# Kernel tuning notes

Measured on AMD Instinct MI355X. Metric: run time of the kernel, lower is better.

Reference implementation:

```python
import jax, jax.numpy as jnp
import numpy as np

N = 50000
E = 800000
IN_F, HID, OUT_F = 512, 256, 64
BN_EPS = 1e-5


def setup_inputs() -> dict:
    key = jax.random.key(0)
    ks = jax.random.split(key, 8)
    x = jax.random.normal(ks[0], (N, IN_F), dtype=jnp.float32)
    edge_rows = jax.random.randint(ks[1], (E,), 0, N, dtype=jnp.int32)
    edge_cols = jax.random.randint(ks[2], (E,), 0, N, dtype=jnp.int32)
    edge_vals = jax.random.uniform(ks[3], (E,), dtype=jnp.float32)
    # xavier_uniform for weights, zeros for biases (as in the torch module)
    lim1 = float(np.sqrt(6.0 / (IN_F + HID)))
    lim2 = float(np.sqrt(6.0 / (HID + OUT_F)))
    W1 = jax.random.uniform(ks[4], (IN_F, HID), minval=-lim1, maxval=lim1, dtype=jnp.float32)
    b1 = jnp.zeros((HID,), dtype=jnp.float32)
    W2 = jax.random.uniform(ks[5], (HID, OUT_F), minval=-lim2, maxval=lim2, dtype=jnp.float32)
    b2 = jnp.zeros((OUT_F,), dtype=jnp.float32)
    # BatchNorm affine params (torch defaults: weight=1, bias=0)
    gamma1 = jnp.ones((HID,), dtype=jnp.float32)
    beta1 = jnp.zeros((HID,), dtype=jnp.float32)
    gamma2 = jnp.ones((OUT_F,), dtype=jnp.float32)
    beta2 = jnp.zeros((OUT_F,), dtype=jnp.float32)
    return dict(x=x, edge_rows=edge_rows, edge_cols=edge_cols, edge_vals=edge_vals,
                W1=W1, b1=b1, gamma1=gamma1, beta1=beta1,
                W2=W2, b2=b2, gamma2=gamma2, beta2=beta2)


def _spmm(rows, cols, vals, dense):
    # sparse [N,N] @ dense [N,F] via gather + segment-sum scatter
    msgs = vals[:, None] * dense[cols]            # [E, F]
    return jax.ops.segment_sum(msgs, rows, num_segments=N)


def _batchnorm(h, gamma, beta):
    # training-mode BatchNorm1d: batch statistics over nodes (biased var)
    mean = jnp.mean(h, axis=0)
    var = jnp.var(h, axis=0)
    return gamma * (h - mean) * jax.lax.rsqrt(var + BN_EPS) + beta


def reference(x, edge_rows, edge_cols, edge_vals,
              W1, b1, gamma1, beta1, W2, b2, gamma2, beta2):
    # layer 1: GCN conv -> BN -> ReLU (dropout is identity in eval / reference)
    h = _spmm(edge_rows, edge_cols, edge_vals, x @ W1) + b1
    h = jax.nn.relu(_batchnorm(h, gamma1, beta1))
    # layer 2: GCN conv -> BN -> log_softmax over classes
    h = _spmm(edge_rows, edge_cols, edge_vals, h @ W2) + b2
    h = _batchnorm(h, gamma2, beta2)
    return jax.nn.log_softmax(h, axis=1)
```

## Files before the change

kernel.cpp:

```cpp
#include <hip/hip_runtime.h>

typedef __attribute__((ext_vector_type(8))) short short8;
typedef __attribute__((ext_vector_type(4))) float f32x4;
typedef __attribute__((ext_vector_type(8))) unsigned short ushort8;

__device__ __forceinline__ unsigned short f2bf(float f) {
  unsigned int u = __builtin_bit_cast(unsigned int, f);
  u += 0x7fffu + ((u >> 16) & 1u);
  return (unsigned short)(u >> 16);
}
__device__ __forceinline__ float bf2f(unsigned short b) {
  return __builtin_bit_cast(float, ((unsigned int)b) << 16);
}
__device__ __forceinline__ void gload_lds16(const void* g, void* l) {
  __builtin_amdgcn_global_load_lds(
      (const __attribute__((address_space(1))) void*)g,
      (__attribute__((address_space(3))) void*)l, 16, 0, 0);
}

__global__ __launch_bounds__(256) void cvt_w1t(
    const float* __restrict__ W1, unsigned short* __restrict__ W1T)
{
  int idx = blockIdx.x * 256 + threadIdx.x;
  int n = idx >> 9, k = idx & 511;
  W1T[idx] = f2bf(W1[(size_t)k * 256 + n]);
}

__global__ __launch_bounds__(256) void cvt_w2t(
    const float* __restrict__ W2, unsigned short* __restrict__ W2T)
{
  int idx = blockIdx.x * 256 + threadIdx.x;
  int n = idx >> 8, k = idx & 255;
  W2T[idx] = f2bf(W2[(size_t)k * 64 + n]);
}

__global__ __launch_bounds__(256) void gemm1_mfma(
    const float* __restrict__ x,
    const unsigned short* __restrict__ w1t,
    unsigned short* __restrict__ H1,
    int M)
{
  __shared__ unsigned short As[2][64 * 64];
  __shared__ unsigned short Bs[2][256 * 64];
  const int tid = threadIdx.x;
  const int wid = tid >> 6, lane = tid & 63;
  const int wc = wid;
  const int m0 = blockIdx.x * 64;

  const int srow = tid >> 3;
  const int ls = ((tid & 7) ^ (srow & 7)) * 8;
  const unsigned short* gB = &w1t[(size_t)srow * 512 + ls];

  const int ar0 = tid >> 3;
  const int ar1 = ar0 + 32;
  const int ac  = tid & 7;
  const int arow0 = m0 + ar0;
  const int arow1 = m0 + ar1;

  float4 a0lo, a0hi, a1lo, a1hi;

  auto loadA = [&](int k0) {
    a0lo = make_float4(0.f, 0.f, 0.f, 0.f); a0hi = a0lo; a1lo = a0lo; a1hi = a0lo;
    if (arow0 < M) {
      a0lo = *(const float4*)&x[(size_t)arow0 * 512 + k0 + ac * 8];
      a0hi = *(const float4*)&x[(size_t)arow0 * 512 + k0 + ac * 8 + 4];
    }
    if (arow1 < M) {
      a1lo = *(const float4*)&x[(size_t)arow1 * 512 + k0 + ac * 8];
      a1hi = *(const float4*)&x[(size_t)arow1 * 512 + k0 + ac * 8 + 4];
    }
  };
  auto writeA = [&](int buf) {
    float v0[8] = {a0lo.x, a0lo.y, a0lo.z, a0lo.w, a0hi.x, a0hi.y, a0hi.z, a0hi.w};
    float v1[8] = {a1lo.x, a1lo.y, a1lo.z, a1lo.w, a1hi.x, a1hi.y, a1hi.z, a1hi.w};
    ushort8 o0, o1;
#pragma unroll
    for (int j = 0; j < 8; ++j) { o0[j] = f2bf(v0[j]); o1[j] = f2bf(v1[j]); }
    *(ushort8*)((char*)As[buf] + ar0 * 128 + ((ac ^ (ar0 & 7)) * 16)) = o0;
    *(ushort8*)((char*)As[buf] + ar1 * 128 + ((ac ^ (ar1 & 7)) * 16)) = o1;
  };
  auto stageB = [&](int k0, int buf) {
    char* lB = (char*)Bs[buf] + (size_t)wid * 1024;
#pragma unroll
    for (int i = 0; i < 8; ++i)
      gload_lds16(gB + (size_t)i * 32 * 512 + k0, lB + (size_t)i * 4096);
  };

  f32x4 acc[4][4] = {};

  loadA(0);
  stageB(0, 0);
  writeA(0);
  __syncthreads();

  for (int kt = 0; kt < 8; ++kt) {
    const int cur = kt & 1, nxt = cur ^ 1;
    if (kt < 7) {
      loadA((kt + 1) * 64);
      stageB((kt + 1) * 64, nxt);
    }
#pragma unroll
    for (int kk = 0; kk < 2; ++kk) {
      short8 a[4], b[4];
#pragma unroll
      for (int m = 0; m < 4; ++m) {
        int row = m * 16 + (lane & 15);
        int phys = (kk * 4 + (lane >> 4)) ^ (row & 7);
        a[m] = *(const short8*)((const char*)As[cur] + row * 128 + phys * 16);
      }
#pragma unroll
      for (int n = 0; n < 4; ++n) {
        int col = wc * 64 + n * 16 + (lane & 15);
        int phys = (kk * 4 + (lane >> 4)) ^ (col & 7);
        b[n] = *(const short8*)((const char*)Bs[cur] + col * 128 + phys * 16);
      }
#pragma unroll
      for (int m = 0; m < 4; ++m)
#pragma unroll
        for (int n = 0; n < 4; ++n)
          acc[m][n] = __builtin_amdgcn_mfma_f32_16x16x32_bf16(a[m], b[n], acc[m][n], 0, 0, 0);
    }
    if (kt < 7) writeA(nxt);
    __syncthreads();
  }

  const int colbase = wc * 64 + (lane & 15);
#pragma unroll
  for (int m = 0; m < 4; ++m) {
    int rowbase = m0 + m * 16 + (lane >> 4) * 4;
#pragma unroll
    for (int j = 0; j < 4; ++j) {
      int row = rowbase + j;
      if (row < M) {
#pragma unroll
        for (int n = 0; n < 4; ++n)
          H1[(size_t)row * 256 + colbase + n * 16] = f2bf(acc[m][n][j]);
      }
    }
  }
}

__global__ __launch_bounds__(256) void gemm2_mfma(
    const unsigned short* __restrict__ A,
    const unsigned short* __restrict__ w2t,
    const float* __restrict__ scsh,
    unsigned short* __restrict__ H2,
    int M)
{
  __shared__ unsigned short As[128 * 64];
  __shared__ unsigned short Bs[64 * 64];
  const int tid = threadIdx.x;
  const int wid = tid >> 6, lane = tid & 63;
  const int wr = wid >> 1, wc = wid & 1;
  const int m0 = blockIdx.x * 128;

  const int srow = tid >> 3;
  const int ls = ((tid & 7) ^ (srow & 7)) * 8;
  const unsigned short* gB = &w2t[(size_t)srow * 256 + ls];
  char* lB = (char*)Bs + (size_t)wid * 1024;

  f32x4 acc[4][2] = {};

  for (int kt = 0; kt < 4; ++kt) {
    const int k0 = kt * 64;
#pragma unroll
    for (int i = 0; i < 2; ++i)
      gload_lds16(gB + (size_t)i * 32 * 256 + k0, lB + (size_t)i * 4096);
#pragma unroll
    for (int i = 0; i < 4; ++i) {
      int chunk = tid + 256 * i;
      int r = chunk >> 3, c = chunk & 7;
      int gk = k0 + c * 8;
      ushort8 u = *(const ushort8*)&A[(size_t)(m0 + r) * 256 + gk];
      float4 sc0 = *(const float4*)&scsh[gk];
      float4 sc1 = *(const float4*)&scsh[gk + 4];
      float4 sh0 = *(const float4*)&scsh[256 + gk];
      float4 sh1 = *(const float4*)&scsh[256 + gk + 4];
      ushort8 o;
      o[0] = f2bf(fmaxf(bf2f(u[0]) * sc0.x + sh0.x, 0.f));
      o[1] = f2bf(fmaxf(bf2f(u[1]) * sc0.y + sh0.y, 0.f));
      o[2] = f2bf(fmaxf(bf2f(u[2]) * sc0.z + sh0.z, 0.f));
      o[3] = f2bf(fmaxf(bf2f(u[3]) * sc0.w + sh0.w, 0.f));
      o[4] = f2bf(fmaxf(bf2f(u[4]) * sc1.x + sh1.x, 0.f));
      o[5] = f2bf(fmaxf(bf2f(u[5]) * sc1.y + sh1.y, 0.f));
      o[6] = f2bf(fmaxf(bf2f(u[6]) * sc1.z + sh1.z, 0.f));
      o[7] = f2bf(fmaxf(bf2f(u[7]) * sc1.w + sh1.w, 0.f));
      *(ushort8*)((char*)As + r * 128 + ((c ^ (r & 7)) * 16)) = o;
    }
    __syncthreads();

#pragma unroll
    for (int kk = 0; kk < 2; ++kk) {
      short8 a[4], b[2];
#pragma unroll
      for (int m = 0; m < 4; ++m) {
        int row = wr * 64 + m * 16 + (lane & 15);
        int phys = (kk * 4 + (lane >> 4)) ^ (row & 7);
        a[m] = *(const short8*)((const char*)As + row * 128 + phys * 16);
      }
#pragma unroll
      for (int n = 0; n < 2; ++n) {
        int col = wc * 32 + n * 16 + (lane & 15);
        int phys = (kk * 4 + (lane >> 4)) ^ (col & 7);
        b[n] = *(const short8*)((const char*)Bs + col * 128 + phys * 16);
      }
#pragma unroll
      for (int m = 0; m < 4; ++m)
#pragma unroll
        for (int n = 0; n < 2; ++n)
          acc[m][n] = __builtin_amdgcn_mfma_f32_16x16x32_bf16(a[m], b[n], acc[m][n], 0, 0, 0);
    }
    __syncthreads();
  }

  const int colbase = wc * 32 + (lane & 15);
#pragma unroll
  for (int m = 0; m < 4; ++m) {
    int rowbase = m0 + wr * 64 + m * 16 + (lane >> 4) * 4;
#pragma unroll
    for (int j = 0; j < 4; ++j) {
      int row = rowbase + j;
      if (row < M) {
#pragma unroll
        for (int n = 0; n < 2; ++n)
          H2[(size_t)row * 64 + colbase + n * 16] = f2bf(acc[m][n][j]);
      }
    }
  }
}

__global__ __launch_bounds__(256) void edge_hist(
    const int* __restrict__ rows, int* __restrict__ cnt, int E)
{
  int e = blockIdx.x * 256 + threadIdx.x;
  if (e < E) atomicAdd(&cnt[rows[e]], 1);
}

__global__ __launch_bounds__(256) void scan_blocksum(
    const int* __restrict__ cnt, int* __restrict__ bsum, int Nrows)
{
  int i = blockIdx.x * 256 + threadIdx.x;
  int v = (i < Nrows) ? cnt[i] : 0;
#pragma unroll
  for (int off = 1; off < 64; off <<= 1) v += __shfl_xor(v, off);
  __shared__ int wsum[4];
  if ((threadIdx.x & 63) == 0) wsum[threadIdx.x >> 6] = v;
  __syncthreads();
  if (threadIdx.x == 0)
    bsum[blockIdx.x] = wsum[0] + wsum[1] + wsum[2] + wsum[3];
}

__global__ __launch_bounds__(256) void scan_boff(
    const int* __restrict__ bsum, int* __restrict__ boff, int NB)
{
  __shared__ int lds[256];
  int t = threadIdx.x;
  int v = (t < NB) ? bsum[t] : 0;
  lds[t] = v;
  __syncthreads();
  for (int off = 1; off < 256; off <<= 1) {
    int u = (t >= off) ? lds[t - off] : 0;
    __syncthreads();
    lds[t] += u;
    __syncthreads();
  }
  boff[t] = (t == 0) ? 0 : lds[t - 1];
}

__global__ __launch_bounds__(256) void scan_write(
    const int* __restrict__ cnt, const int* __restrict__ boff,
    int* __restrict__ rowptr, int* __restrict__ cursor, int Nrows, int E)
{
  __shared__ int lds[256];
  int t = threadIdx.x;
  int i = blockIdx.x * 256 + t;
  int v = (i < Nrows) ? cnt[i] : 0;
  lds[t] = v;
  __syncthreads();
  for (int off = 1; off < 256; off <<= 1) {
    int u = (t >= off) ? lds[t - off] : 0;
    __syncthreads();
    lds[t] += u;
    __syncthreads();
  }
  int excl = boff[blockIdx.x] + lds[t] - v;
  if (i < Nrows) { rowptr[i] = excl; cursor[i] = excl; }
  if (i == Nrows) rowptr[i] = E;
}

__global__ __launch_bounds__(256) void edge_scatter(
    const int* __restrict__ rows, const int* __restrict__ cols,
    const float* __restrict__ vals, int* __restrict__ cursor,
    int2* __restrict__ spack, int E)
{
  int e = blockIdx.x * 256 + threadIdx.x;
  if (e < E) {
    int r = rows[e];
    int p = atomicAdd(&cursor[r], 1);
    spack[p] = make_int2(cols[e], __float_as_int(vals[e]));
  }
}

__global__ __launch_bounds__(256) void spmm_gather_bf(
    const int* __restrict__ rowptr, const int2* __restrict__ sp,
    const unsigned short* __restrict__ D,
    unsigned short* __restrict__ out, int Nrows)
{
  const int lane = threadIdx.x & 63;
  const int r = blockIdx.x * 4 + (threadIdx.x >> 6);
  if (r >= Nrows) return;
  const int s = rowptr[r], e = rowptr[r + 1];
  float4 acc0 = make_float4(0.f, 0.f, 0.f, 0.f);
  float4 acc1 = make_float4(0.f, 0.f, 0.f, 0.f);
  int j = s;
  for (; j + 3 < e; j += 4) {
    int2 p0 = sp[j], p1 = sp[j + 1], p2 = sp[j + 2], p3 = sp[j + 3];
    ushort4 d0 = *(const ushort4*)&D[(size_t)p0.x * 256 + lane * 4];
    ushort4 d1 = *(const ushort4*)&D[(size_t)p1.x * 256 + lane * 4];
    ushort4 d2 = *(const ushort4*)&D[(size_t)p2.x * 256 + lane * 4];
    ushort4 d3 = *(const ushort4*)&D[(size_t)p3.x * 256 + lane * 4];
    float v0 = __int_as_float(p0.y), v1 = __int_as_float(p1.y);
    float v2 = __int_as_float(p2.y), v3 = __int_as_float(p3.y);
    acc0.x = fmaf(v0, bf2f(d0.x), acc0.x); acc0.y = fmaf(v0, bf2f(d0.y), acc0.y);
    acc0.z = fmaf(v0, bf2f(d0.z), acc0.z); acc0.w = fmaf(v0, bf2f(d0.w), acc0.w);
    acc1.x = fmaf(v1, bf2f(d1.x), acc1.x); acc1.y = fmaf(v1, bf2f(d1.y), acc1.y);
    acc1.z = fmaf(v1, bf2f(d1.z), acc1.z); acc1.w = fmaf(v1, bf2f(d1.w), acc1.w);
    acc0.x = fmaf(v2, bf2f(d2.x), acc0.x); acc0.y = fmaf(v2, bf2f(d2.y), acc0.y);
    acc0.z = fmaf(v2, bf2f(d2.z), acc0.z); acc0.w = fmaf(v2, bf2f(d2.w), acc0.w);
    acc1.x = fmaf(v3, bf2f(d3.x), acc1.x); acc1.y = fmaf(v3, bf2f(d3.y), acc1.y);
    acc1.z = fmaf(v3, bf2f(d3.z), acc1.z); acc1.w = fmaf(v3, bf2f(d3.w), acc1.w);
  }
  for (; j < e; ++j) {
    int2 p = sp[j];
    float v = __int_as_float(p.y);
    ushort4 d = *(const ushort4*)&D[(size_t)p.x * 256 + lane * 4];
    acc0.x = fmaf(v, bf2f(d.x), acc0.x); acc0.y = fmaf(v, bf2f(d.y), acc0.y);
    acc0.z = fmaf(v, bf2f(d.z), acc0.z); acc0.w = fmaf(v, bf2f(d.w), acc0.w);
  }
  ushort4 ov;
  ov.x = f2bf(acc0.x + acc1.x); ov.y = f2bf(acc0.y + acc1.y);
  ov.z = f2bf(acc0.z + acc1.z); ov.w = f2bf(acc0.w + acc1.w);
  *(ushort4*)&out[(size_t)r * 256 + lane * 4] = ov;
}

__global__ __launch_bounds__(256) void spmm_gather_bf64(
    const int* __restrict__ rowptr, const int2* __restrict__ sp,
    const unsigned short* __restrict__ D,
    float* __restrict__ out, int Nrows)
{
  const int lane = threadIdx.x & 63;
  const int r = blockIdx.x * 4 + (threadIdx.x >> 6);
  if (r >= Nrows) return;
  const int s = rowptr[r], e = rowptr[r + 1];
  float acc0 = 0.f, acc1 = 0.f;
  int j = s;
  for (; j + 3 < e; j += 4) {
    int2 p0 = sp[j], p1 = sp[j + 1], p2 = sp[j + 2], p3 = sp[j + 3];
    float d0 = bf2f(D[(size_t)p0.x * 64 + lane]);
    float d1 = bf2f(D[(size_t)p1.x * 64 + lane]);
    float d2 = bf2f(D[(size_t)p2.x * 64 + lane]);
    float d3 = bf2f(D[(size_t)p3.x * 64 + lane]);
    acc0 = fmaf(__int_as_float(p0.y), d0, acc0);
    acc1 = fmaf(__int_as_float(p1.y), d1, acc1);
    acc0 = fmaf(__int_as_float(p2.y), d2, acc0);
    acc1 = fmaf(__int_as_float(p3.y), d3, acc1);
  }
  for (; j < e; ++j) {
    int2 p = sp[j];
    acc0 = fmaf(__int_as_float(p.y), bf2f(D[(size_t)p.x * 64 + lane]), acc0);
  }
  out[(size_t)r * 64 + lane] = acc0 + acc1;
}

__global__ __launch_bounds__(256) void bn_stats_bf256(
    const unsigned short* __restrict__ H, float* __restrict__ partials, int Nrows)
{
  const int cc = threadIdx.x & 31;
  const int c = cc * 8;
  const int rr = threadIdx.x >> 5;
  float s[8] = {}, q[8] = {};
  for (int r = blockIdx.x * 8 + rr; r < Nrows; r += gridDim.x * 8) {
    ushort8 u = *(const ushort8*)&H[(size_t)r * 256 + c];
#pragma unroll
    for (int j = 0; j < 8; ++j) {
      float f = bf2f(u[j]);
      s[j] += f; q[j] += f * f;
    }
  }
  __shared__ float lds[256][16];
  float* L = lds[threadIdx.x];
#pragma unroll
  for (int j = 0; j < 8; ++j) { L[j] = s[j]; L[8 + j] = q[j]; }
  __syncthreads();
  if (rr == 0) {
#pragma unroll
    for (int r2 = 1; r2 < 8; ++r2) {
      float* Mm = lds[cc + r2 * 32];
#pragma unroll
      for (int j = 0; j < 8; ++j) { s[j] += Mm[j]; q[j] += Mm[8 + j]; }
    }
    float* P = &partials[(size_t)blockIdx.x * 512];
#pragma unroll
    for (int j = 0; j < 8; ++j) { P[c + j] = s[j]; P[256 + c + j] = q[j]; }
  }
}

__global__ __launch_bounds__(256) void bn_stats64(
    const float* __restrict__ H, float* __restrict__ partials, int Nrows)
{
  const int cc = threadIdx.x % 16;
  const int c = cc * 4;
  const int rr = threadIdx.x / 16;
  float4 s = make_float4(0.f, 0.f, 0.f, 0.f);
  float4 q = make_float4(0.f, 0.f, 0.f, 0.f);
  for (int r = blockIdx.x * 16 + rr; r < Nrows; r += gridDim.x * 16) {
    float4 v = *(const float4*)&H[(size_t)r * 64 + c];
    s.x += v.x; s.y += v.y; s.z += v.z; s.w += v.w;
    q.x += v.x * v.x; q.y += v.y * v.y; q.z += v.z * v.z; q.w += v.w * v.w;
  }
  __shared__ float lds[256][8];
  float* L = lds[threadIdx.x];
  L[0] = s.x; L[1] = s.y; L[2] = s.z; L[3] = s.w;
  L[4] = q.x; L[5] = q.y; L[6] = q.z; L[7] = q.w;
  __syncthreads();
  if (rr == 0) {
#pragma unroll
    for (int r2 = 1; r2 < 16; ++r2) {
      float* Mm = lds[cc + r2 * 16];
      s.x += Mm[0]; s.y += Mm[1]; s.z += Mm[2]; s.w += Mm[3];
      q.x += Mm[4]; q.y += Mm[5]; q.z += Mm[6]; q.w += Mm[7];
    }
    float* P = &partials[(size_t)blockIdx.x * 128];
    *(float4*)&P[c] = s;
    *(float4*)&P[64 + c] = q;
  }
}

template<int C>
__global__ __launch_bounds__(256) void bn_finalize_par(
    const float* __restrict__ partials,
    const float* __restrict__ gamma, const float* __restrict__ beta,
    float* __restrict__ scsh, int G, float invN)
{
  const int c = blockIdx.x;
  const int t = threadIdx.x;
  float sum = 0.f, sq = 0.f;
  for (int g = t; g < G; g += 256) {
    sum += partials[(size_t)g * 2 * C + c];
    sq  += partials[(size_t)g * 2 * C + C + c];
  }
#pragma unroll
  for (int off = 1; off < 64; off <<= 1) {
    sum += __shfl_xor(sum, off);
    sq  += __shfl_xor(sq, off);
  }
  __shared__ float ws[4][2];
  if ((t & 63) == 0) { ws[t >> 6][0] = sum; ws[t >> 6][1] = sq; }
  __syncthreads();
  if (t == 0) {
    sum = ws[0][0] + ws[1][0] + ws[2][0] + ws[3][0];
    sq  = ws[0][1] + ws[1][1] + ws[2][1] + ws[3][1];
    float mean = sum * invN;
    float var = sq * invN - mean * mean;
    float rstd = rsqrtf(var + 1e-5f);
    float sc = gamma[c] * rstd;
    scsh[c] = sc;
    scsh[C + c] = beta[c] - mean * sc;
  }
}

__global__ __launch_bounds__(256) void bn_lsm(
    const float* __restrict__ H, const float* __restrict__ scsh,
    float* __restrict__ out, int Nrows)
{
  int lane = threadIdx.x & 63;
  int r = blockIdx.x * 4 + (threadIdx.x >> 6);
  if (r >= Nrows) return;
  float y = H[(size_t)r * 64 + lane] * scsh[lane] + scsh[64 + lane];
  float m = y;
#pragma unroll
  for (int off = 32; off >= 1; off >>= 1) m = fmaxf(m, __shfl_xor(m, off));
  float ex = expf(y - m);
  float s = ex;
#pragma unroll
  for (int off = 32; off >= 1; off >>= 1) s += __shfl_xor(s, off);
  out[(size_t)r * 64 + lane] = (y - m) - logf(s);
}

extern "C" void kernel_launch(void* const* d_in, const int* in_sizes, int n_in,
                              void* d_out, int out_size, void* d_ws, size_t ws_size,
                              hipStream_t stream) {
  const float* x      = (const float*)d_in[0];
  const int*   erow   = (const int*)  d_in[1];
  const int*   ecol   = (const int*)  d_in[2];
  const float* eval   = (const float*)d_in[3];
  const float* W1     = (const float*)d_in[4];
  const float* gamma1 = (const float*)d_in[6];
  const float* beta1  = (const float*)d_in[7];
  const float* W2     = (const float*)d_in[8];
  const float* gamma2 = (const float*)d_in[10];
  const float* beta2  = (const float*)d_in[11];

  const int N = in_sizes[0] / 512;
  const int E = in_sizes[1];

  char* ws = (char*)d_ws;
  unsigned short* H1b   = (unsigned short*)(ws + 0);
  float* partials1      = (float*)(ws + 0);
  unsigned short* H2b   = (unsigned short*)(ws + 0);
  float* H2AGG          = (float*)(ws + 12800000);
  unsigned short* H1AGGb= (unsigned short*)(ws + 51200000);
  float* partials2      = (float*)(ws + 51200000);
  unsigned short* w1t   = (unsigned short*)(ws + 76865536);
  float* scsh1          = (float*)(ws + 77127680);
  float* scsh2          = (float*)(ws + 77129728);
  int*   rowptr         = (int*)(ws + 77130240);
  int*   cnt            = (int*)(ws + 77330244);
  int*   cursor         = (int*)(ws + 77530244);
  int2*  spack          = (int2*)(ws + 77730248);
  int*   bsum           = (int*)(ws + 84130248);
  int*   boff           = (int*)(ws + 84131272);
  unsigned short* w2t   = (unsigned short*)(ws + 84132352);

  hipMemsetAsync(cnt, 0, (size_t)N * 4, stream);

  const dim3 blk(256);
  const int eblocks = (E + 255) / 256;
  const int NB = (N + 255) / 256;

  edge_hist<<<eblocks, blk, 0, stream>>>(erow, cnt, E);
  scan_blocksum<<<NB, blk, 0, stream>>>(cnt, bsum, N);
  scan_boff<<<1, blk, 0, stream>>>(bsum, boff, NB);
  scan_write<<<NB + 1, blk, 0, stream>>>(cnt, boff, rowptr, cursor, N, E);
  edge_scatter<<<eblocks, blk, 0, stream>>>(erow, ecol, eval, cursor, spack, E);

  cvt_w1t<<<512, blk, 0, stream>>>(W1, w1t);
  cvt_w2t<<<64, blk, 0, stream>>>(W2, w2t);

  gemm1_mfma<<<(N + 63) / 64, blk, 0, stream>>>(x, w1t, H1b, N);
  spmm_gather_bf<<<(N + 3) / 4, blk, 0, stream>>>(rowptr, spack, H1b, H1AGGb, N);
  bn_stats_bf256<<<256, blk, 0, stream>>>(H1AGGb, partials1, N);
  bn_finalize_par<256><<<256, blk, 0, stream>>>(partials1, gamma1, beta1, scsh1, 256, 1.0f / N);
  gemm2_mfma<<<(N + 127) / 128, blk, 0, stream>>>(H1AGGb, w2t, scsh1, H2b, N);
  spmm_gather_bf64<<<(N + 3) / 4, blk, 0, stream>>>(rowptr, spack, H2b, H2AGG, N);
  bn_stats64<<<256, blk, 0, stream>>>(H2AGG, partials2, N);
  bn_finalize_par<64><<<64, blk, 0, stream>>>(partials2, gamma2, beta2, scsh2, 256, 1.0f / N);
  bn_lsm<<<(N + 3) / 4, blk, 0, stream>>>(H2AGG, scsh2, (float*)d_out, N);
}
```

Measured before the change: 274.8 us.

## Halve GEMM1 K-tile, deepen SpMM gather unroll, merge weight conversion kernels

The first GEMM now uses 32-wide K tiles with halved LDS buffers, a 4-way XOR swizzle, and simpler B staging over 16 iterations. This aims to cut LDS use and raise occupancy, at the cost of more barriers per tile. Both SpMM gather kernels issue eight independent row loads per iteration instead of four, to keep more gathers in flight. The two weight transpose and convert kernels are merged into one launch to save launch overhead.

```diff
diff --git a/kernel.cpp b/kernel.cpp
--- a/kernel.cpp
+++ b/kernel.cpp
@@ -18,20 +18,19 @@
       (__attribute__((address_space(3))) void*)l, 16, 0, 0);
 }
 
-__global__ __launch_bounds__(256) void cvt_w1t(
-    const float* __restrict__ W1, unsigned short* __restrict__ W1T)
+__global__ __launch_bounds__(256) void cvt_weights(
+    const float* __restrict__ W1, const float* __restrict__ W2,
+    unsigned short* __restrict__ w1t, unsigned short* __restrict__ w2t)
 {
   int idx = blockIdx.x * 256 + threadIdx.x;
-  int n = idx >> 9, k = idx & 511;
-  W1T[idx] = f2bf(W1[(size_t)k * 256 + n]);
-}
-
-__global__ __launch_bounds__(256) void cvt_w2t(
-    const float* __restrict__ W2, unsigned short* __restrict__ W2T)
-{
-  int idx = blockIdx.x * 256 + threadIdx.x;
-  int n = idx >> 8, k = idx & 255;
-  W2T[idx] = f2bf(W2[(size_t)k * 64 + n]);
+  if (idx < 131072) {
+    int n = idx >> 9, k = idx & 511;
+    w1t[idx] = f2bf(W1[(size_t)k * 256 + n]);
+  } else if (idx < 131072 + 16384) {
+    int i = idx - 131072;
+    int n = i >> 8, k = i & 255;
+    w2t[i] = f2bf(W2[(size_t)k * 64 + n]);
+  }
 }
 
 __global__ __launch_bounds__(256) void gemm1_mfma(
@@ -40,50 +39,43 @@
     unsigned short* __restrict__ H1,
     int M)
 {
-  __shared__ unsigned short As[2][64 * 64];
-  __shared__ unsigned short Bs[2][256 * 64];
+  __shared__ unsigned short As[2][64 * 32];
+  __shared__ unsigned short Bs[2][256 * 32];
   const int tid = threadIdx.x;
   const int wid = tid >> 6, lane = tid & 63;
   const int wc = wid;
   const int m0 = blockIdx.x * 64;
 
-  const int srow = tid >> 3;
-  const int ls = ((tid & 7) ^ (srow & 7)) * 8;
-  const unsigned short* gB = &w1t[(size_t)srow * 512 + ls];
-
-  const int ar0 = tid >> 3;
-  const int ar1 = ar0 + 32;
-  const int ac  = tid & 7;
-  const int arow0 = m0 + ar0;
-  const int arow1 = m0 + ar1;
-
-  float4 a0lo, a0hi, a1lo, a1hi;
-
+  const int ar = tid >> 2;
+  const int ac = tid & 3;
+  const int arow = m0 + ar;
+  const int aphys = ac ^ ((ar >> 1) & 3);
+
+  const int bq = lane >> 2;
+  const int bslotx = (lane & 3) ^ ((lane >> 3) & 3);
+
+  float4 alo, ahi;
   auto loadA = [&](int k0) {
-    a0lo = make_float4(0.f, 0.f, 0.f, 0.f); a0hi = a0lo; a1lo = a0lo; a1hi = a0lo;
-    if (arow0 < M) {
-      a0lo = *(const float4*)&x[(size_t)arow0 * 512 + k0 + ac * 8];
-      a0hi = *(const float4*)&x[(size_t)arow0 * 512 + k0 + ac * 8 + 4];
-    }
-    if (arow1 < M) {
-      a1lo = *(const float4*)&x[(size_t)arow1 * 512 + k0 + ac * 8];
-      a1hi = *(const float4*)&x[(size_t)arow1 * 512 + k0 + ac * 8 + 4];
+    alo = make_float4(0.f, 0.f, 0.f, 0.f); ahi = alo;
+    if (arow < M) {
+      alo = *(const float4*)&x[(size_t)arow * 512 + k0 + ac * 8];
+      ahi = *(const float4*)&x[(size_t)arow * 512 + k0 + ac * 8 + 4];
     }
   };
   auto writeA = [&](int buf) {
-    float v0[8] = {a0lo.x, a0lo.y, a0lo.z, a0lo.w, a0hi.x, a0hi.y, a0hi.z, a0hi.w};
-    float v1[8] = {a1lo.x, a1lo.y, a1lo.z, a1lo.w, a1hi.x, a1hi.y, a1hi.z, a1hi.w};
-    ushort8 o0, o1;
-#pragma unroll
-    for (int j = 0; j < 8; ++j) { o0[j] = f2bf(v0[j]); o1[j] = f2bf(v1[j]); }
-    *(ushort8*)((char*)As[buf] + ar0 * 128 + ((ac ^ (ar0 & 7)) * 16)) = o0;
-    *(ushort8*)((char*)As[buf] + ar1 * 128 + ((ac ^ (ar1 & 7)) * 16)) = o1;
+    ushort8 o;
+    o[0] = f2bf(alo.x); o[1] = f2bf(alo.y); o[2] = f2bf(alo.z); o[3] = f2bf(alo.w);
+    o[4] = f2bf(ahi.x); o[5] = f2bf(ahi.y); o[6] = f2bf(ahi.z); o[7] = f2bf(ahi.w);
+    *(ushort8*)((char*)As[buf] + ar * 64 + aphys * 16) = o;
   };
   auto stageB = [&](int k0, int buf) {
-    char* lB = (char*)Bs[buf] + (size_t)wid * 1024;
-#pragma unroll
-    for (int i = 0; i < 8; ++i)
-      gload_lds16(gB + (size_t)i * 32 * 512 + k0, lB + (size_t)i * 4096);
+#pragma unroll
+    for (int i = 0; i < 4; ++i) {
+      int g = wid + 4 * i;
+      int col = g * 16 + bq;
+      gload_lds16(&w1t[(size_t)col * 512 + k0 + bslotx * 8],
+                  (char*)Bs[buf] + g * 1024);
+    }
   };
 
   f32x4 acc[4][4] = {};
@@ -93,34 +85,31 @@
   writeA(0);
   __syncthreads();
 
-  for (int kt = 0; kt < 8; ++kt) {
+  for (int kt = 0; kt < 16; ++kt) {
     const int cur = kt & 1, nxt = cur ^ 1;
-    if (kt < 7) {
-      loadA((kt + 1) * 64);
-      stageB((kt + 1) * 64, nxt);
-    }
-#pragma unroll
-    for (int kk = 0; kk < 2; ++kk) {
-      short8 a[4], b[4];
-#pragma unroll
-      for (int m = 0; m < 4; ++m) {
-        int row = m * 16 + (lane & 15);
-        int phys = (kk * 4 + (lane >> 4)) ^ (row & 7);
-        a[m] = *(const short8*)((const char*)As[cur] + row * 128 + phys * 16);
-      }
-#pragma unroll
-      for (int n = 0; n < 4; ++n) {
-        int col = wc * 64 + n * 16 + (lane & 15);
-        int phys = (kk * 4 + (lane >> 4)) ^ (col & 7);
-        b[n] = *(const short8*)((const char*)Bs[cur] + col * 128 + phys * 16);
-      }
-#pragma unroll
-      for (int m = 0; m < 4; ++m)
-#pragma unroll
-        for (int n = 0; n < 4; ++n)
-          acc[m][n] = __builtin_amdgcn_mfma_f32_16x16x32_bf16(a[m], b[n], acc[m][n], 0, 0, 0);
-    }
-    if (kt < 7) writeA(nxt);
+    if (kt < 15) {
+      loadA((kt + 1) * 32);
+      stageB((kt + 1) * 32, nxt);
+    }
+    short8 a[4], b[4];
+#pragma unroll
+    for (int m = 0; m < 4; ++m) {
+      int row = m * 16 + (lane & 15);
+      int phys = (lane >> 4) ^ ((row >> 1) & 3);
+      a[m] = *(const short8*)((const char*)As[cur] + row * 64 + phys * 16);
+    }
+#pragma unroll
+    for (int n = 0; n < 4; ++n) {
+      int col = wc * 64 + n * 16 + (lane & 15);
+      int phys = (lane >> 4) ^ ((col >> 1) & 3);
+      b[n] = *(const short8*)((const char*)Bs[cur] + col * 64 + phys * 16);
+    }
+#pragma unroll
+    for (int m = 0; m < 4; ++m)
+#pragma unroll
+      for (int n = 0; n < 4; ++n)
+        acc[m][n] = __builtin_amdgcn_mfma_f32_16x16x32_bf16(a[m], b[n], acc[m][n], 0, 0, 0);
+    if (kt < 15) writeA(nxt);
     __syncthreads();
   }
 
@@ -313,24 +302,34 @@
   float4 acc0 = make_float4(0.f, 0.f, 0.f, 0.f);
   float4 acc1 = make_float4(0.f, 0.f, 0.f, 0.f);
   int j = s;
-  for (; j + 3 < e; j += 4) {
-    int2 p0 = sp[j], p1 = sp[j + 1], p2 = sp[j + 2], p3 = sp[j + 3];
+  for (; j + 7 < e; j += 8) {
+    int2 p[8];
+    ushort4 d[8];
+#pragma unroll
+    for (int t = 0; t < 8; ++t) p[t] = sp[j + t];
+#pragma unroll
+    for (int t = 0; t < 8; ++t)
+      d[t] = *(const ushort4*)&D[(size_t)p[t].x * 256 + lane * 4];
+#pragma unroll
+    for (int t = 0; t < 8; t += 2) {
+      float v0 = __int_as_float(p[t].y), v1 = __int_as_float(p[t + 1].y);
+      acc0.x = fmaf(v0, bf2f(d[t].x), acc0.x); acc0.y = fmaf(v0, bf2f(d[t].y), acc0.y);
+      acc0.z = fmaf(v0, bf2f(d[t].z), acc0.z); acc0.w = fmaf(v0, bf2f(d[t].w), acc0.w);
+      acc1.x = fmaf(v1, bf2f(d[t + 1].x), acc1.x); acc1.y = fmaf(v1, bf2f(d[t + 1].y), acc1.y);
+      acc1.z = fmaf(v1, bf2f(d[t + 1].z), acc1.z); acc1.w = fmaf(v1, bf2f(d[t + 1].w), acc1.w);
+    }
+  }
+  for (; j + 1 < e; j += 2) {
+    int2 p0 = sp[j], p1 = sp[j + 1];
     ushort4 d0 = *(const ushort4*)&D[(size_t)p0.x * 256 + lane * 4];
     ushort4 d1 = *(const ushort4*)&D[(size_t)p1.x * 256 + lane * 4];
-    ushort4 d2 = *(const ushort4*)&D[(size_t)p2.x * 256 + lane * 4];
-    ushort4 d3 = *(const ushort4*)&D[(size_t)p3.x * 256 + lane * 4];
     float v0 = __int_as_float(p0.y), v1 = __int_as_float(p1.y);
-    float v2 = __int_as_float(p2.y), v3 = __int_as_float(p3.y);
     acc0.x = fmaf(v0, bf2f(d0.x), acc0.x); acc0.y = fmaf(v0, bf2f(d0.y), acc0.y);
     acc0.z = fmaf(v0, bf2f(d0.z), acc0.z); acc0.w = fmaf(v0, bf2f(d0.w), acc0.w);
     acc1.x = fmaf(v1, bf2f(d1.x), acc1.x); acc1.y = fmaf(v1, bf2f(d1.y), acc1.y);
     acc1.z = fmaf(v1, bf2f(d1.z), acc1.z); acc1.w = fmaf(v1, bf2f(d1.w), acc1.w);
-    acc0.x = fmaf(v2, bf2f(d2.x), acc0.x); acc0.y = fmaf(v2, bf2f(d2.y), acc0.y);
-    acc0.z = fmaf(v2, bf2f(d2.z), acc0.z); acc0.w = fmaf(v2, bf2f(d2.w), acc0.w);
-    acc1.x = fmaf(v3, bf2f(d3.x), acc1.x); acc1.y = fmaf(v3, bf2f(d3.y), acc1.y);
-    acc1.z = fmaf(v3, bf2f(d3.z), acc1.z); acc1.w = fmaf(v3, bf2f(d3.w), acc1.w);
-  }
-  for (; j < e; ++j) {
+  }
+  if (j < e) {
     int2 p = sp[j];
     float v = __int_as_float(p.y);
     ushort4 d = *(const ushort4*)&D[(size_t)p.x * 256 + lane * 4];
@@ -354,16 +353,18 @@
   const int s = rowptr[r], e = rowptr[r + 1];
   float acc0 = 0.f, acc1 = 0.f;
   int j = s;
-  for (; j + 3 < e; j += 4) {
-    int2 p0 = sp[j], p1 = sp[j + 1], p2 = sp[j + 2], p3 = sp[j + 3];
-    float d0 = bf2f(D[(size_t)p0.x * 64 + lane]);
-    float d1 = bf2f(D[(size_t)p1.x * 64 + lane]);
-    float d2 = bf2f(D[(size_t)p2.x * 64 + lane]);
-    float d3 = bf2f(D[(size_t)p3.x * 64 + lane]);
-    acc0 = fmaf(__int_as_float(p0.y), d0, acc0);
-    acc1 = fmaf(__int_as_float(p1.y), d1, acc1);
-    acc0 = fmaf(__int_as_float(p2.y), d2, acc0);
-    acc1 = fmaf(__int_as_float(p3.y), d3, acc1);
+  for (; j + 7 < e; j += 8) {
+    int2 p[8];
+    float d[8];
+#pragma unroll
+    for (int t = 0; t < 8; ++t) p[t] = sp[j + t];
+#pragma unroll
+    for (int t = 0; t < 8; ++t) d[t] = bf2f(D[(size_t)p[t].x * 64 + lane]);
+#pragma unroll
+    for (int t = 0; t < 8; t += 2) {
+      acc0 = fmaf(__int_as_float(p[t].y), d[t], acc0);
+      acc1 = fmaf(__int_as_float(p[t + 1].y), d[t + 1], acc1);
+    }
   }
   for (; j < e; ++j) {
     int2 p = sp[j];
@@ -534,8 +535,7 @@
   scan_write<<<NB + 1, blk, 0, stream>>>(cnt, boff, rowptr, cursor, N, E);
   edge_scatter<<<eblocks, blk, 0, stream>>>(erow, ecol, eval, cursor, spack, E);
 
-  cvt_w1t<<<512, blk, 0, stream>>>(W1, w1t);
-  cvt_w2t<<<64, blk, 0, stream>>>(W2, w2t);
+  cvt_weights<<<576, blk, 0, stream>>>(W1, W2, w1t, w2t);
 
   gemm1_mfma<<<(N + 63) / 64, blk, 0, stream>>>(x, w1t, H1b, N);
   spmm_gather_bf<<<(N + 3) / 4, blk, 0, stream>>>(rowptr, spack, H1b, H1AGGb, N);
```

New measurement: 273.8 us. No clear change (-0.3%).
